# Optimization experiments

Measured on AMD Instinct MI355X. Metric: run time of the kernel, lower is better.

## Reference

```python
import jax, jax.numpy as jnp
import numpy as np

EMB = 1024
NH = 16
HS = EMB // NH

def setup_inputs() -> dict:
    key = jax.random.key(0)
    ks = jax.random.split(key, 9)
    s = 0.02
    x = jax.random.normal(ks[0], (4, 2048, EMB), dtype=jnp.float32)
    Wq = jax.random.normal(ks[1], (EMB, EMB), dtype=jnp.float32) * s
    bq = jnp.zeros((EMB,), jnp.float32)
    Wk = jax.random.normal(ks[2], (EMB, EMB), dtype=jnp.float32) * s
    bk = jnp.zeros((EMB,), jnp.float32)
    Wv = jax.random.normal(ks[3], (EMB, EMB), dtype=jnp.float32) * s
    bv = jnp.zeros((EMB,), jnp.float32)
    Wo = jax.random.normal(ks[4], (EMB, EMB), dtype=jnp.float32) * s
    bo = jnp.zeros((EMB,), jnp.float32)
    return {"x": x, "Wq": Wq, "bq": bq, "Wk": Wk, "bk": bk,
            "Wv": Wv, "bv": bv, "Wo": Wo, "bo": bo}

def reference(x, Wq, bq, Wk, bk, Wv, bv, Wo, bo):
    B, T, C = x.shape
    q = x @ Wq + bq
    k = x @ Wk + bk
    v = x @ Wv + bv
    # [B, H, T, hs]
    q = q.reshape(B, T, NH, HS).transpose(0, 2, 1, 3)
    k = k.reshape(B, T, NH, HS).transpose(0, 2, 1, 3)
    v = v.reshape(B, T, NH, HS).transpose(0, 2, 1, 3)
    scale = 1.0 / np.sqrt(HS).astype(np.float32)
    att = jnp.einsum('bhqd,bhkd->bhqk', q, k) * scale
    causal = jnp.tril(jnp.ones((T, T), dtype=bool))
    att = jnp.where(causal[None, None], att, jnp.float32(-jnp.inf))
    att = jax.nn.softmax(att, axis=-1)
    y = jnp.einsum('bhqk,bhkd->bhqd', att, v)
    y = y.transpose(0, 2, 1, 3).reshape(B, T, C)
    return y @ Wo + bo
```

## Files before the change

kernel.cpp:

```cpp
#include <hip/hip_runtime.h>

#define EMB   1024
#define NHEAD 16
#define HS    64
#define BATCH 4
#define SEQ   2048
#define MTOK  (BATCH*SEQ)

typedef __bf16 bf16;
typedef __bf16 bf16x8 __attribute__((ext_vector_type(8)));
typedef __bf16 bf16x4 __attribute__((ext_vector_type(4)));
typedef float  f32x4  __attribute__((ext_vector_type(4)));
typedef _Float16 f16;
typedef f16 f16x4 __attribute__((ext_vector_type(4)));
typedef f16 f16x8 __attribute__((ext_vector_type(8)));

#define MFMA16(a,b,c)     __builtin_amdgcn_mfma_f32_16x16x32_bf16(a,b,c,0,0,0)
#define MFMA_H32(a,b,c)   __builtin_amdgcn_mfma_f32_16x16x32_f16(a,b,c,0,0,0)
#define MFMA_H16(a,b,c)   __builtin_amdgcn_mfma_f32_16x16x16f16(a,b,c,0,0,0)

#if __has_builtin(__builtin_amdgcn_exp2f)
#define EXP2(x) __builtin_amdgcn_exp2f(x)
#else
#define EXP2(x) exp2f(x)
#endif

#define GLL(g, l) __builtin_amdgcn_global_load_lds(                         \
        (const __attribute__((address_space(1))) void*)(g),                 \
        (__attribute__((address_space(3))) void*)(l), 16, 0, 0)

__global__ __launch_bounds__(256) void k_prep(
        const float* __restrict__ x, bf16* __restrict__ xb,
        const float* __restrict__ W0, const float* __restrict__ W1,
        const float* __restrict__ W2, const float* __restrict__ W3,
        bf16* __restrict__ T0, bf16* __restrict__ T1,
        bf16* __restrict__ T2, bf16* __restrict__ T3) {
    const int z = blockIdx.z;
    if (z == 0) {
        const int blk = blockIdx.y * 16 + blockIdx.x;
        const size_t base = (size_t)blk * 32768;
        for (int j = threadIdx.x; j < 8192; j += 256) {
            size_t i = base + (size_t)j * 4;
            float4 v = *(const float4*)(x + i);
            bf16x4 o;
            o[0] = (bf16)v.x; o[1] = (bf16)v.y; o[2] = (bf16)v.z; o[3] = (bf16)v.w;
            *(bf16x4*)(xb + i) = o;
        }
        return;
    }
    __shared__ float tile[64][65];
    const float* W = (z == 1) ? W0 : (z == 2) ? W1 : (z == 3) ? W2 : W3;
    bf16* Wt = (z == 1) ? T0 : (z == 2) ? T1 : (z == 3) ? T2 : T3;
    int c0 = blockIdx.x * 64, r0 = blockIdx.y * 64;
    int tx = threadIdx.x & 63, ty = threadIdx.x >> 6;
    #pragma unroll
    for (int r = ty; r < 64; r += 4)
        tile[r][tx] = W[(r0 + r) * EMB + c0 + tx];
    __syncthreads();
    #pragma unroll
    for (int cc = ty; cc < 64; cc += 4)
        Wt[(c0 + cc) * EMB + r0 + tx] = (bf16)tile[tx][cc];
}

__global__ __launch_bounds__(512, 2) void k_qkv_gemm(
        const bf16* __restrict__ xb,
        const bf16* __restrict__ Wqt, const bf16* __restrict__ Wkt, const bf16* __restrict__ Wvt,
        const float* __restrict__ bq, const float* __restrict__ bk, const float* __restrict__ bv,
        f16* __restrict__ Q, f16* __restrict__ K, f16* __restrict__ Vt) {
    __shared__ __align__(16) bf16 As[4][8192];
    __shared__ __align__(16) bf16 Bs[4][8192];
    const int tid = threadIdx.x;
    const int lane = tid & 63;
    const int wave = tid >> 6;
    const int l15 = lane & 15, quad = lane >> 4;
    const int wm = wave >> 2;
    const int wn = wave & 3;

    const int bid = blockIdx.x;
    const int swz = (bid & 7) * 48 + (bid >> 3);
    const int mt = swz & 31;
    const int nt = swz >> 5;
    const int which = nt >> 2;
    const int n0 = (nt & 3) * 256;

    const bf16* Wt   = (which == 0) ? Wqt : (which == 1) ? Wkt : Wvt;
    const float* bias = (which == 0) ? bq : (which == 1) ? bk : bv;

    f32x4 acc[8][4];
    #pragma unroll
    for (int i = 0; i < 8; i++)
        #pragma unroll
        for (int j = 0; j < 4; j++) acc[i][j] = (f32x4){0.f, 0.f, 0.f, 0.f};

    const int P  = tid >> 3, s8 = tid & 7;
    const int c  = s8 ^ (P & 7);
    const int r_ = 2 * P + (c >> 2);
    const int kc = c & 3;
    const bf16* Asrc = xb + (size_t)(mt * 256 + r_) * EMB + kc * 8;
    const bf16* Bsrc = Wt + (size_t)(n0 + r_) * EMB + kc * 8;

#define QSTAGE(t, q) do {                                                   \
        GLL(Asrc + (t) * 32,                 &As[q][tid * 8]);              \
        GLL(Asrc + 128 * EMB + (t) * 32,     &As[q][tid * 8 + 4096]);       \
        GLL(Bsrc + (t) * 32,                 &Bs[q][tid * 8]);              \
        GLL(Bsrc + 128 * EMB + (t) * 32,     &Bs[q][tid * 8 + 4096]); } while (0)

    int aoff[8], boff[4];
    #pragma unroll
    for (int mf = 0; mf < 8; mf++) {
        int row = wm * 128 + mf * 16 + l15;
        int p = row >> 1;
        int slot = (((row & 1) << 2) | quad) ^ (p & 7);
        aoff[mf] = p * 64 + slot * 8;
    }
    #pragma unroll
    for (int nf = 0; nf < 4; nf++) {
        int row = wn * 64 + nf * 16 + l15;
        int p = row >> 1;
        int slot = (((row & 1) << 2) | quad) ^ (p & 7);
        boff[nf] = p * 64 + slot * 8;
    }

    QSTAGE(0, 0);
    QSTAGE(1, 1);

    #pragma unroll
    for (int t = 0; t < 32; t++) {
        if (t < 31) asm volatile("s_waitcnt vmcnt(4)" ::: "memory");
        else        asm volatile("s_waitcnt vmcnt(0)" ::: "memory");
        __builtin_amdgcn_s_barrier();
        asm volatile("" ::: "memory");

        const bf16* Ab = As[t & 3];
        const bf16* Bb = Bs[t & 3];
        bf16x8 a[8], b[4];
        #pragma unroll
        for (int mf = 0; mf < 8; mf++) a[mf] = *(const bf16x8*)(Ab + aoff[mf]);
        #pragma unroll
        for (int nf = 0; nf < 4; nf++) b[nf] = *(const bf16x8*)(Bb + boff[nf]);

        if (t + 2 < 32) QSTAGE(t + 2, (t + 2) & 3);

        __builtin_amdgcn_s_setprio(1);
        #pragma unroll
        for (int mf = 0; mf < 8; mf++)
            #pragma unroll
            for (int nf = 0; nf < 4; nf++)
                acc[mf][nf] = MFMA16(a[mf], b[nf], acc[mf][nf]);
        __builtin_amdgcn_s_setprio(0);
    }
#undef QSTAGE

    const float QSCALE = 0.18033688011112043f;
    #pragma unroll
    for (int nf = 0; nf < 4; nf++) {
        const int col = n0 + wn * 64 + nf * 16 + l15;
        const float bv_ = bias[col];
        const int h = col >> 6, d = col & 63;
        #pragma unroll
        for (int mf = 0; mf < 8; mf++) {
            #pragma unroll
            for (int r = 0; r < 4; r++) {
                const int row = mt * 256 + wm * 128 + mf * 16 + quad * 4 + r;
                const int b_ = row >> 11, tk = row & (SEQ - 1);
                const float val = acc[mf][nf][r] + bv_;
                if (which == 0) {
                    Q[((size_t)(b_ * NHEAD + h) * SEQ + tk) * HS + d] = (f16)(val * QSCALE);
                } else if (which == 1) {
                    K[((size_t)(b_ * NHEAD + h) * SEQ + tk) * HS + d] = (f16)val;
                } else {
                    Vt[(((size_t)(b_ * NHEAD + h) * 32 + (tk >> 6)) * 64 + d) * 64 + (tk & 63)] = (f16)val;
                }
            }
        }
    }
}

__global__ __launch_bounds__(256) void k_attn(
        const f16* __restrict__ Q, const f16* __restrict__ K,
        const f16* __restrict__ Vt, bf16* __restrict__ y) {
    __shared__ __align__(16) f16 kbuf[2][64 * 64];
    __shared__ __align__(16) f16 vbuf[2][64 * 64];
    const int tid = threadIdx.x;
    const int wave = tid >> 6, lane = tid & 63;
    const int l15 = lane & 15, quad = lane >> 4;
    const int qtA = blockIdx.x;
    const int bh = blockIdx.y;
    const int h = bh & (NHEAD - 1), b_ = bh >> 4;

    const f16* Qb = Q + (size_t)bh * SEQ * HS;
    const f16* Kb = K + (size_t)bh * SEQ * HS;
    const f16* Vb = Vt + (size_t)bh * 32 * 4096;

    const int c0 = tid, c1 = tid + 256;
    const int soff0 = (c0 >> 3) * 64 + (((c0 & 7) ^ ((c0 >> 3) & 7)) * 8);
    const int soff1 = (c1 >> 3) * 64 + (((c1 & 7) ^ ((c1 >> 3) & 7)) * 8);
    const int swz = l15 & 7;

    f16x4 ones;
    #pragma unroll
    for (int i = 0; i < 4; i++) ones[i] = (f16)1.0f;

    #pragma unroll 1
    for (int phase = 0; phase < 2; ++phase) {
        const int qt = phase ? (15 - qtA) : qtA;
        const int ntiles = 2 * qt + 2;
        const int qrow0 = qt * 128 + wave * 32;

        f16x8 qb[2][2];
        #pragma unroll
        for (int qf = 0; qf < 2; qf++)
            #pragma unroll
            for (int dk = 0; dk < 2; dk++)
                qb[qf][dk] = *(const f16x8*)(Qb + (qrow0 + 16 * qf + l15) * HS + 32 * dk + quad * 8);

        f32x4 o[2][4], lacc[2];
        #pragma unroll
        for (int qf = 0; qf < 2; qf++) {
            lacc[qf] = (f32x4){0.f, 0.f, 0.f, 0.f};
            #pragma unroll
            for (int df = 0; df < 4; df++) o[qf][df] = (f32x4){0.f, 0.f, 0.f, 0.f};
        }

        f16x8 kr0 = *(const f16x8*)(Kb + c0 * 8);
        f16x8 kr1 = *(const f16x8*)(Kb + c1 * 8);
        f16x8 vr0 = *(const f16x8*)(Vb + c0 * 8);
        f16x8 vr1 = *(const f16x8*)(Vb + c1 * 8);
        __syncthreads();
        *(f16x8*)(kbuf[0] + soff0) = kr0;
        *(f16x8*)(kbuf[0] + soff1) = kr1;
        *(f16x8*)(vbuf[0] + soff0) = vr0;
        *(f16x8*)(vbuf[0] + soff1) = vr1;

        for (int it = 0; it < ntiles; ++it) {
            const int kv0 = it * 64;
            __syncthreads();
            if (it + 1 < ntiles) {
                const f16* kg = Kb + (size_t)(kv0 + 64) * HS;
                const f16* vg = Vb + (size_t)(it + 1) * 4096;
                kr0 = *(const f16x8*)(kg + c0 * 8);
                kr1 = *(const f16x8*)(kg + c1 * 8);
                vr0 = *(const f16x8*)(vg + c0 * 8);
                vr1 = *(const f16x8*)(vg + c1 * 8);
            }
            if (kv0 <= qrow0 + 31) {
                const f16* kb_ = kbuf[it & 1];
                const f16* vb_ = vbuf[it & 1];

                f32x4 s[4][2];
                #pragma unroll
                for (int mb = 0; mb < 4; mb++) {
                    f16x8 ka0 = *(const f16x8*)(kb_ + (16 * mb + l15) * 64 + ((quad ^ swz) * 8));
                    f16x8 ka1 = *(const f16x8*)(kb_ + (16 * mb + l15) * 64 + (((4 + quad) ^ swz) * 8));
                    #pragma unroll
                    for (int qf = 0; qf < 2; qf++) {
                        f32x4 t = (f32x4){0.f, 0.f, 0.f, 0.f};
                        t = MFMA_H32(ka0, qb[qf][0], t);
                        t = MFMA_H32(ka1, qb[qf][1], t);
                        s[mb][qf] = t;
                    }
                }

                f16x4 pa[4][2];
                const bool edge = (kv0 + 63 > qrow0);
                #pragma unroll
                for (int mb = 0; mb < 4; mb++)
                    #pragma unroll
                    for (int qf = 0; qf < 2; qf++) {
                        f16x4 p;
                        if (edge) {
                            #pragma unroll
                            for (int r = 0; r < 4; r++) {
                                const int kvc = kv0 + 16 * mb + quad * 4 + r;
                                const int qq  = qrow0 + 16 * qf + l15;
                                p[r] = (f16)((kvc <= qq) ? EXP2(s[mb][qf][r]) : 0.f);
                            }
                        } else {
                            #pragma unroll
                            for (int r = 0; r < 4; r++)
                                p[r] = (f16)EXP2(s[mb][qf][r]);
                        }
                        pa[mb][qf] = p;
                    }

                #pragma unroll
                for (int df = 0; df < 4; df++)
                    #pragma unroll
                    for (int kb = 0; kb < 4; kb++) {
                        f16x4 vfrag = *(const f16x4*)(vb_ + (16 * df + l15) * 64 +
                                        (((2 * kb + (quad >> 1)) ^ swz) * 8) + (quad & 1) * 4);
                        #pragma unroll
                        for (int qf = 0; qf < 2; qf++)
                            o[qf][df] = MFMA_H16(pa[kb][qf], vfrag, o[qf][df]);
                    }
                #pragma unroll
                for (int kb = 0; kb < 4; kb++)
                    #pragma unroll
                    for (int qf = 0; qf < 2; qf++)
                        lacc[qf] = MFMA_H16(pa[kb][qf], ones, lacc[qf]);
            }
            if (it + 1 < ntiles) {
                const int nb = (it + 1) & 1;
                *(f16x8*)(kbuf[nb] + soff0) = kr0;
                *(f16x8*)(kbuf[nb] + soff1) = kr1;
                *(f16x8*)(vbuf[nb] + soff0) = vr0;
                *(f16x8*)(vbuf[nb] + soff1) = vr1;
            }
        }

        #pragma unroll
        for (int qf = 0; qf < 2; qf++)
            #pragma unroll
            for (int r = 0; r < 4; r++) {
                float inv = 1.f / lacc[qf][r];
                int t = qrow0 + 16 * qf + quad * 4 + r;
                bf16* yp = y + ((size_t)(b_ * SEQ + t)) * EMB + h * HS;
                #pragma unroll
                for (int df = 0; df < 4; df++)
                    yp[df * 16 + l15] = (bf16)(o[qf][df][r] * inv);
            }
    }
}

__global__ __launch_bounds__(256) void k_out_gemm(
        const bf16* __restrict__ y, const bf16* __restrict__ Wot,
        const float* __restrict__ bo, float* __restrict__ out) {
    __shared__ __align__(16) bf16 As[128 * 64];
    __shared__ __align__(16) bf16 Bs[128 * 64];
    const int tid = threadIdx.x;
    const int lane = tid & 63;
    const int wave = tid >> 6;
    const int l15 = lane & 15, quad = lane >> 4;
    const int wm = (wave >> 1) * 64, wn = (wave & 1) * 64;
    const int m0 = blockIdx.x * 128;
    const int n0 = blockIdx.y * 128;

    f32x4 acc[4][4];
    #pragma unroll
    for (int i = 0; i < 4; i++)
        #pragma unroll
        for (int j = 0; j < 4; j++) acc[i][j] = (f32x4){0.f, 0.f, 0.f, 0.f};

    const int r0_ = tid >> 3;
    const int kcs = ((tid & 7) ^ (r0_ & 7)) * 8;
    const bf16* Ag = y   + (size_t)m0 * EMB + r0_ * EMB + kcs;
    const bf16* Bg = Wot + (size_t)n0 * EMB + r0_ * EMB + kcs;
    const int rsw = l15 & 7;

    for (int k0 = 0; k0 < EMB; k0 += 64) {
        __syncthreads();
        #pragma unroll
        for (int g = 0; g < 4; g++) {
            GLL(Ag + 32 * g * EMB + k0, As + (tid + g * 256) * 8);
            GLL(Bg + 32 * g * EMB + k0, Bs + (tid + g * 256) * 8);
        }
        __syncthreads();

        bf16x8 af[2][4], bfr[2][4];
        #pragma unroll
        for (int h = 0; h < 2; h++) {
            #pragma unroll
            for (int rf = 0; rf < 4; rf++)
                af[h][rf] = *(const bf16x8*)(As + (wm + rf * 16 + l15) * 64 +
                                             (((4 * h + quad) ^ rsw) * 8));
            #pragma unroll
            for (int cf = 0; cf < 4; cf++)
                bfr[h][cf] = *(const bf16x8*)(Bs + (wn + cf * 16 + l15) * 64 +
                                              (((4 * h + quad) ^ rsw) * 8));
        }
        #pragma unroll
        for (int h = 0; h < 2; h++)
            #pragma unroll
            for (int rf = 0; rf < 4; rf++)
                #pragma unroll
                for (int cf = 0; cf < 4; cf++)
                    acc[rf][cf] = MFMA16(af[h][rf], bfr[h][cf], acc[rf][cf]);
    }

    #pragma unroll
    for (int cf = 0; cf < 4; cf++) {
        const int col = n0 + wn + cf * 16 + l15;
        const float bv_ = bo[col];
        #pragma unroll
        for (int rf = 0; rf < 4; rf++) {
            #pragma unroll
            for (int r = 0; r < 4; r++) {
                const int row = m0 + wm + rf * 16 + quad * 4 + r;
                out[(size_t)row * EMB + col] = acc[rf][cf][r] + bv_;
            }
        }
    }
}

extern "C" void kernel_launch(void* const* d_in, const int* in_sizes, int n_in,
                              void* d_out, int out_size, void* d_ws, size_t ws_size,
                              hipStream_t stream) {
    const float* x  = (const float*)d_in[0];
    const float* Wq = (const float*)d_in[1];
    const float* bq = (const float*)d_in[2];
    const float* Wk = (const float*)d_in[3];
    const float* bk = (const float*)d_in[4];
    const float* Wv = (const float*)d_in[5];
    const float* bv = (const float*)d_in[6];
    const float* Wo = (const float*)d_in[7];
    const float* bo = (const float*)d_in[8];
    float* out = (float*)d_out;

    char* ws = (char*)d_ws;
    bf16* xb  = (bf16*)(ws);
    bf16* Wqt = (bf16*)(ws + (16u << 20));
    bf16* Wkt = (bf16*)(ws + (18u << 20));
    bf16* Wvt = (bf16*)(ws + (20u << 20));
    bf16* Wot = (bf16*)(ws + (22u << 20));
    f16*  Q   = (f16*)(ws + (24u << 20));
    f16*  K   = (f16*)(ws + (40u << 20));
    f16*  Vt  = (f16*)(ws + (56u << 20));
    bf16* y   = (bf16*)(ws + (72u << 20));

    dim3 gp(16, 16, 5);
    k_prep<<<gp, 256, 0, stream>>>(x, xb, Wq, Wk, Wv, Wo, Wqt, Wkt, Wvt, Wot);

    dim3 g1(384);
    k_qkv_gemm<<<g1, 512, 0, stream>>>(xb, Wqt, Wkt, Wvt, bq, bk, bv, Q, K, Vt);

    dim3 g2(SEQ / 256, BATCH * NHEAD);
    k_attn<<<g2, 256, 0, stream>>>(Q, K, Vt, y);

    dim3 g3(MTOK / 128, EMB / 128);
    k_out_gemm<<<g3, 256, 0, stream>>>(y, Wot, bo, out);
}
```

Baseline: 322.9 us.

## Restructure QKV GEMM main loop into K=64 windows with interleaved MFMA/LDS schedule

The QKV projection GEMM now stages 64-wide K slices in a double buffer instead of 32-wide slices in a four-deep ring. Each window splits LDS fragment loads and MFMA groups into phases separated by barriers, priority hints and sched_barriers, with A and B prefetches issued at different points. The swizzled 1D grid becomes a plain 2D grid, and the V-transposed epilogue writes 4-element vectors instead of scalar stores. The aim is better overlap of global loads, LDS reads and matrix ops. The costs are more barriers per K step and the loss of the L2-friendly block swizzle.

```diff
diff --git a/kernel.cpp b/kernel.cpp
--- a/kernel.cpp
+++ b/kernel.cpp
@@ -67,89 +67,105 @@
         const bf16* __restrict__ Wqt, const bf16* __restrict__ Wkt, const bf16* __restrict__ Wvt,
         const float* __restrict__ bq, const float* __restrict__ bk, const float* __restrict__ bv,
         f16* __restrict__ Q, f16* __restrict__ K, f16* __restrict__ Vt) {
-    __shared__ __align__(16) bf16 As[4][8192];
-    __shared__ __align__(16) bf16 Bs[4][8192];
+    __shared__ __align__(16) bf16 As[2][256 * 64];
+    __shared__ __align__(16) bf16 Bs[2][256 * 64];
     const int tid = threadIdx.x;
     const int lane = tid & 63;
+    const int l15 = lane & 15, quad = lane >> 4;
     const int wave = tid >> 6;
-    const int l15 = lane & 15, quad = lane >> 4;
     const int wm = wave >> 2;
     const int wn = wave & 3;
 
-    const int bid = blockIdx.x;
-    const int swz = (bid & 7) * 48 + (bid >> 3);
-    const int mt = swz & 31;
-    const int nt = swz >> 5;
+    const int mt = blockIdx.x;
+    const int nt = blockIdx.y;
     const int which = nt >> 2;
     const int n0 = (nt & 3) * 256;
 
     const bf16* Wt   = (which == 0) ? Wqt : (which == 1) ? Wkt : Wvt;
     const float* bias = (which == 0) ? bq : (which == 1) ? bk : bv;
 
+    const bf16* Abase = xb + (size_t)mt * 256 * EMB;
+    const bf16* Bbase = Wt + (size_t)n0 * EMB;
+
+    const int srow = tid >> 3;
+    const int sc8  = ((tid & 7) ^ (srow & 7)) * 8;
+    const int sdst = srow * 64 + (tid & 7) * 8;
+
+    const int arow = (wm * 128 + l15) * 64;
+    const int brow = (wn * 64 + l15) * 64;
+    const int k7 = l15 & 7;
+    const int ksl0 = ((quad) ^ k7) * 8;
+    const int ksl1 = ((4 + quad) ^ k7) * 8;
+
     f32x4 acc[8][4];
     #pragma unroll
     for (int i = 0; i < 8; i++)
         #pragma unroll
         for (int j = 0; j < 4; j++) acc[i][j] = (f32x4){0.f, 0.f, 0.f, 0.f};
 
-    const int P  = tid >> 3, s8 = tid & 7;
-    const int c  = s8 ^ (P & 7);
-    const int r_ = 2 * P + (c >> 2);
-    const int kc = c & 3;
-    const bf16* Asrc = xb + (size_t)(mt * 256 + r_) * EMB + kc * 8;
-    const bf16* Bsrc = Wt + (size_t)(n0 + r_) * EMB + kc * 8;
-
-#define QSTAGE(t, q) do {                                                   \
-        GLL(Asrc + (t) * 32,                 &As[q][tid * 8]);              \
-        GLL(Asrc + 128 * EMB + (t) * 32,     &As[q][tid * 8 + 4096]);       \
-        GLL(Bsrc + (t) * 32,                 &Bs[q][tid * 8]);              \
-        GLL(Bsrc + 128 * EMB + (t) * 32,     &Bs[q][tid * 8 + 4096]); } while (0)
-
-    int aoff[8], boff[4];
-    #pragma unroll
-    for (int mf = 0; mf < 8; mf++) {
-        int row = wm * 128 + mf * 16 + l15;
-        int p = row >> 1;
-        int slot = (((row & 1) << 2) | quad) ^ (p & 7);
-        aoff[mf] = p * 64 + slot * 8;
-    }
-    #pragma unroll
-    for (int nf = 0; nf < 4; nf++) {
-        int row = wn * 64 + nf * 16 + l15;
-        int p = row >> 1;
-        int slot = (((row & 1) << 2) | quad) ^ (p & 7);
-        boff[nf] = p * 64 + slot * 8;
-    }
-
-    QSTAGE(0, 0);
-    QSTAGE(1, 1);
-
-    #pragma unroll
-    for (int t = 0; t < 32; t++) {
-        if (t < 31) asm volatile("s_waitcnt vmcnt(4)" ::: "memory");
-        else        asm volatile("s_waitcnt vmcnt(0)" ::: "memory");
-        __builtin_amdgcn_s_barrier();
-        asm volatile("" ::: "memory");
-
-        const bf16* Ab = As[t & 3];
-        const bf16* Bb = Bs[t & 3];
-        bf16x8 a[8], b[4];
-        #pragma unroll
-        for (int mf = 0; mf < 8; mf++) a[mf] = *(const bf16x8*)(Ab + aoff[mf]);
-        #pragma unroll
-        for (int nf = 0; nf < 4; nf++) b[nf] = *(const bf16x8*)(Bb + boff[nf]);
-
-        if (t + 2 < 32) QSTAGE(t + 2, (t + 2) & 3);
-
-        __builtin_amdgcn_s_setprio(1);
-        #pragma unroll
-        for (int mf = 0; mf < 8; mf++)
-            #pragma unroll
-            for (int nf = 0; nf < 4; nf++)
-                acc[mf][nf] = MFMA16(a[mf], b[nf], acc[mf][nf]);
-        __builtin_amdgcn_s_setprio(0);
-    }
-#undef QSTAGE
+#define STAGE_A(T, cb) do { const int ko = (T) * 64;                          \
+    GLL(Abase + (size_t)(srow      ) * EMB + ko + sc8, &As[cb][sdst        ]);\
+    GLL(Abase + (size_t)(srow +  64) * EMB + ko + sc8, &As[cb][sdst + 4096 ]);\
+    GLL(Abase + (size_t)(srow + 128) * EMB + ko + sc8, &As[cb][sdst + 8192 ]);\
+    GLL(Abase + (size_t)(srow + 192) * EMB + ko + sc8, &As[cb][sdst + 12288]);\
+} while (0)
+#define STAGE_B(T, cb) do { const int ko = (T) * 64;                          \
+    GLL(Bbase + (size_t)(srow      ) * EMB + ko + sc8, &Bs[cb][sdst        ]);\
+    GLL(Bbase + (size_t)(srow +  64) * EMB + ko + sc8, &Bs[cb][sdst + 4096 ]);\
+    GLL(Bbase + (size_t)(srow + 128) * EMB + ko + sc8, &Bs[cb][sdst + 8192 ]);\
+    GLL(Bbase + (size_t)(srow + 192) * EMB + ko + sc8, &Bs[cb][sdst + 12288]);\
+} while (0)
+
+#define LDA(c_, mf, ks) (*(const bf16x8*)(&As[c_][arow + (mf) * 1024 + (ks)]))
+#define LDB(c_, nf, ks) (*(const bf16x8*)(&Bs[c_][brow + (nf) * 1024 + (ks)]))
+
+#define BARX __builtin_amdgcn_s_barrier()
+#define PRI1 __builtin_amdgcn_s_setprio(1)
+#define PRI0 __builtin_amdgcn_s_setprio(0)
+#define SCHB __builtin_amdgcn_sched_barrier(0)
+#define VM4 asm volatile("s_waitcnt vmcnt(4)" ::: "memory")
+#define VM0 asm volatile("s_waitcnt vmcnt(0)" ::: "memory")
+
+#define MF4(mb, av)                                                          \
+    _Pragma("unroll") for (int i_ = 0; i_ < 4; i_++)                         \
+    _Pragma("unroll") for (int j_ = 0; j_ < 4; j_++)                         \
+        acc[(mb) + i_][j_] = MFMA16(av[i_], br[j_], acc[(mb) + i_][j_])
+
+#define WINDOW(c_, SA, SB, VM) do {                                          \
+    _Pragma("unroll") for (int i = 0; i < 4; i++) ar[i]  = LDA(c_, i,     ksl0);\
+    _Pragma("unroll") for (int j = 0; j < 4; j++) br[j]  = LDB(c_, j,     ksl0);\
+    SA;                                                                      \
+    SCHB;                                                                    \
+    BARX; PRI1; MF4(0, ar);  PRI0; BARX;                                     \
+    _Pragma("unroll") for (int i = 0; i < 4; i++) ar2[i] = LDA(c_, 4 + i, ksl0);\
+    BARX; PRI1; MF4(4, ar2); PRI0; BARX;                                     \
+    _Pragma("unroll") for (int i = 0; i < 4; i++) ar[i]  = LDA(c_, i,     ksl1);\
+    _Pragma("unroll") for (int j = 0; j < 4; j++) br[j]  = LDB(c_, j,     ksl1);\
+    BARX; PRI1; MF4(0, ar);  PRI0; BARX;                                     \
+    _Pragma("unroll") for (int i = 0; i < 4; i++) ar2[i] = LDA(c_, 4 + i, ksl1);\
+    SB;                                                                      \
+    SCHB; VM;                                                                \
+    BARX; PRI1; MF4(4, ar2); PRI0; BARX;                                     \
+} while (0)
+
+    STAGE_A(0, 0); STAGE_B(0, 0); STAGE_B(1, 1);
+    SCHB;
+    VM4;
+    BARX;
+
+    bf16x8 ar[4], br[4], ar2[4];
+    #pragma unroll 2
+    for (int W = 0; W < 14; ++W) {
+        const int c = W & 1;
+        WINDOW(c, STAGE_A(W + 1, c ^ 1), STAGE_B(W + 2, c), VM4);
+    }
+    WINDOW(0, STAGE_A(15, 1), (void)0, VM0);
+    WINDOW(1, (void)0, (void)0, (void)0);
+
+#undef WINDOW
+#undef MF4
+#undef STAGE_A
+#undef STAGE_B
 
     const float QSCALE = 0.18033688011112043f;
     #pragma unroll
@@ -159,18 +175,24 @@
         const int h = col >> 6, d = col & 63;
         #pragma unroll
         for (int mf = 0; mf < 8; mf++) {
-            #pragma unroll
-            for (int r = 0; r < 4; r++) {
-                const int row = mt * 256 + wm * 128 + mf * 16 + quad * 4 + r;
-                const int b_ = row >> 11, tk = row & (SEQ - 1);
-                const float val = acc[mf][nf][r] + bv_;
-                if (which == 0) {
-                    Q[((size_t)(b_ * NHEAD + h) * SEQ + tk) * HS + d] = (f16)(val * QSCALE);
-                } else if (which == 1) {
-                    K[((size_t)(b_ * NHEAD + h) * SEQ + tk) * HS + d] = (f16)val;
-                } else {
-                    Vt[(((size_t)(b_ * NHEAD + h) * 32 + (tk >> 6)) * 64 + d) * 64 + (tk & 63)] = (f16)val;
-                }
+            const int row0 = mt * 256 + wm * 128 + mf * 16 + quad * 4;
+            const int b_ = row0 >> 11, tk0 = row0 & (SEQ - 1);
+            if (which == 0) {
+                #pragma unroll
+                for (int r = 0; r < 4; r++)
+                    Q[((size_t)(b_ * NHEAD + h) * SEQ + (tk0 + r)) * HS + d] =
+                        (f16)((acc[mf][nf][r] + bv_) * QSCALE);
+            } else if (which == 1) {
+                #pragma unroll
+                for (int r = 0; r < 4; r++)
+                    K[((size_t)(b_ * NHEAD + h) * SEQ + (tk0 + r)) * HS + d] =
+                        (f16)(acc[mf][nf][r] + bv_);
+            } else {
+                f16x4 vv;
+                #pragma unroll
+                for (int r = 0; r < 4; r++) vv[r] = (f16)(acc[mf][nf][r] + bv_);
+                *(f16x4*)(Vt + (((size_t)(b_ * NHEAD + h) * 32 + (tk0 >> 6)) * 64 + d) * 64
+                          + (tk0 & 63)) = vv;
             }
         }
     }
@@ -420,7 +442,7 @@
     dim3 gp(16, 16, 5);
     k_prep<<<gp, 256, 0, stream>>>(x, xb, Wq, Wk, Wv, Wo, Wqt, Wkt, Wvt, Wot);
 
-    dim3 g1(384);
+    dim3 g1(32, 12);
     k_qkv_gemm<<<g1, 512, 0, stream>>>(xb, Wqt, Wkt, Wvt, bq, bk, bv, Q, K, Vt);
 
     dim3 g2(SEQ / 256, BATCH * NHEAD);
```

Result: faster. 287.4 us (-11.0%).

## Restructure QKV GEMM pipeline into double-buffered split-phase schedule with vectorized stores

Applied to the files above, without the earlier changes.

Replaces the 4-deep LDS ring (prefetch distance 2) in the QKV GEMM with a 2-buffer scheme. Each k-step is split into two MFMA halves, with the A and B global-to-LDS loads for the next step interleaved between them and separated by barriers and scheduling fences. The swizzled 1D block mapping becomes a plain 2D grid, which may reduce L2 locality. The epilogue is specialized per output: V^T gets vectorized f16x4 stores, and Q/K use a shared scaled path. Less LDS per block could raise occupancy, but the shallower prefetch and full vmcnt(0) waits each step risk exposing memory latency.

```diff
diff --git a/kernel.cpp b/kernel.cpp
--- a/kernel.cpp
+++ b/kernel.cpp
@@ -67,110 +67,154 @@
         const bf16* __restrict__ Wqt, const bf16* __restrict__ Wkt, const bf16* __restrict__ Wvt,
         const float* __restrict__ bq, const float* __restrict__ bk, const float* __restrict__ bv,
         f16* __restrict__ Q, f16* __restrict__ K, f16* __restrict__ Vt) {
-    __shared__ __align__(16) bf16 As[4][8192];
-    __shared__ __align__(16) bf16 Bs[4][8192];
+    __shared__ __align__(16) bf16 As[2][8192];
+    __shared__ __align__(16) bf16 Bs[2][8192];
     const int tid = threadIdx.x;
     const int lane = tid & 63;
+    const int l15 = lane & 15, quad = lane >> 4;
     const int wave = tid >> 6;
-    const int l15 = lane & 15, quad = lane >> 4;
     const int wm = wave >> 2;
     const int wn = wave & 3;
 
-    const int bid = blockIdx.x;
-    const int swz = (bid & 7) * 48 + (bid >> 3);
-    const int mt = swz & 31;
-    const int nt = swz >> 5;
+    const int mt = blockIdx.x;
+    const int nt = blockIdx.y;
     const int which = nt >> 2;
     const int n0 = (nt & 3) * 256;
 
     const bf16* Wt   = (which == 0) ? Wqt : (which == 1) ? Wkt : Wvt;
     const float* bias = (which == 0) ? bq : (which == 1) ? bk : bv;
 
+    const bf16* Abase = xb + (size_t)mt * 256 * EMB;
+    const bf16* Bbase = Wt + (size_t)n0 * EMB;
+
+    const int P   = tid >> 3, s8 = tid & 7;
+    const int cch = s8 ^ (P & 7);
+    const int r_  = 2 * P + (cch >> 2);
+    const int kc8 = (cch & 3) * 8;
+    const bf16* Asrc = Abase + (size_t)r_ * EMB + kc8;
+    const bf16* Bsrc = Bbase + (size_t)r_ * EMB + kc8;
+
+#define STAGE_A(T, cb) do {                                                  \
+    GLL(Asrc + (T) * 32,             &As[cb][tid * 8]);                      \
+    GLL(Asrc + 128 * EMB + (T) * 32, &As[cb][tid * 8 + 4096]); } while (0)
+#define STAGE_B(T, cb) do {                                                  \
+    GLL(Bsrc + (T) * 32,             &Bs[cb][tid * 8]);                      \
+    GLL(Bsrc + 128 * EMB + (T) * 32, &Bs[cb][tid * 8 + 4096]); } while (0)
+
+    int aoff[8], boff[4];
+    #pragma unroll
+    for (int mf = 0; mf < 8; mf++) {
+        const int row = wm * 128 + mf * 16 + l15;
+        const int Pr = row >> 1, hh = row & 1;
+        aoff[mf] = Pr * 64 + ((((hh << 2) | quad)) ^ (Pr & 7)) * 8;
+    }
+    #pragma unroll
+    for (int nf = 0; nf < 4; nf++) {
+        const int row = wn * 64 + nf * 16 + l15;
+        const int Pr = row >> 1, hh = row & 1;
+        boff[nf] = Pr * 64 + ((((hh << 2) | quad)) ^ (Pr & 7)) * 8;
+    }
+
     f32x4 acc[8][4];
     #pragma unroll
     for (int i = 0; i < 8; i++)
         #pragma unroll
         for (int j = 0; j < 4; j++) acc[i][j] = (f32x4){0.f, 0.f, 0.f, 0.f};
 
-    const int P  = tid >> 3, s8 = tid & 7;
-    const int c  = s8 ^ (P & 7);
-    const int r_ = 2 * P + (c >> 2);
-    const int kc = c & 3;
-    const bf16* Asrc = xb + (size_t)(mt * 256 + r_) * EMB + kc * 8;
-    const bf16* Bsrc = Wt + (size_t)(n0 + r_) * EMB + kc * 8;
-
-#define QSTAGE(t, q) do {                                                   \
-        GLL(Asrc + (t) * 32,                 &As[q][tid * 8]);              \
-        GLL(Asrc + 128 * EMB + (t) * 32,     &As[q][tid * 8 + 4096]);       \
-        GLL(Bsrc + (t) * 32,                 &Bs[q][tid * 8]);              \
-        GLL(Bsrc + 128 * EMB + (t) * 32,     &Bs[q][tid * 8 + 4096]); } while (0)
-
-    int aoff[8], boff[4];
-    #pragma unroll
-    for (int mf = 0; mf < 8; mf++) {
-        int row = wm * 128 + mf * 16 + l15;
-        int p = row >> 1;
-        int slot = (((row & 1) << 2) | quad) ^ (p & 7);
-        aoff[mf] = p * 64 + slot * 8;
-    }
-    #pragma unroll
-    for (int nf = 0; nf < 4; nf++) {
-        int row = wn * 64 + nf * 16 + l15;
-        int p = row >> 1;
-        int slot = (((row & 1) << 2) | quad) ^ (p & 7);
-        boff[nf] = p * 64 + slot * 8;
-    }
-
-    QSTAGE(0, 0);
-    QSTAGE(1, 1);
-
-    #pragma unroll
-    for (int t = 0; t < 32; t++) {
-        if (t < 31) asm volatile("s_waitcnt vmcnt(4)" ::: "memory");
-        else        asm volatile("s_waitcnt vmcnt(0)" ::: "memory");
-        __builtin_amdgcn_s_barrier();
-        asm volatile("" ::: "memory");
-
-        const bf16* Ab = As[t & 3];
-        const bf16* Bb = Bs[t & 3];
-        bf16x8 a[8], b[4];
-        #pragma unroll
-        for (int mf = 0; mf < 8; mf++) a[mf] = *(const bf16x8*)(Ab + aoff[mf]);
-        #pragma unroll
-        for (int nf = 0; nf < 4; nf++) b[nf] = *(const bf16x8*)(Bb + boff[nf]);
-
-        if (t + 2 < 32) QSTAGE(t + 2, (t + 2) & 3);
-
-        __builtin_amdgcn_s_setprio(1);
-        #pragma unroll
-        for (int mf = 0; mf < 8; mf++)
-            #pragma unroll
-            for (int nf = 0; nf < 4; nf++)
-                acc[mf][nf] = MFMA16(a[mf], b[nf], acc[mf][nf]);
-        __builtin_amdgcn_s_setprio(0);
-    }
-#undef QSTAGE
+#define BARX __builtin_amdgcn_s_barrier()
+#define PRI1 __builtin_amdgcn_s_setprio(1)
+#define PRI0 __builtin_amdgcn_s_setprio(0)
+#define SCHB __builtin_amdgcn_sched_barrier(0)
+#define VM0 asm volatile("s_waitcnt vmcnt(0)" ::: "memory")
+
+    STAGE_A(0, 0); STAGE_B(0, 0);
+    SCHB; VM0; BARX;
+
+    bf16x8 a[4], b[4], a2[4];
+    #pragma unroll 1
+    for (int W = 0; W < 31; ++W) {
+        const int c = W & 1;
+        const bf16* Ab = As[c];
+        const bf16* Bb = Bs[c];
+        #pragma unroll
+        for (int i = 0; i < 4; i++) a[i] = *(const bf16x8*)(Ab + aoff[i]);
+        #pragma unroll
+        for (int j = 0; j < 4; j++) b[j] = *(const bf16x8*)(Bb + boff[j]);
+        STAGE_A(W + 1, c ^ 1);
+        SCHB;
+        BARX; PRI1;
+        #pragma unroll
+        for (int i = 0; i < 4; i++)
+            #pragma unroll
+            for (int j = 0; j < 4; j++)
+                acc[i][j] = MFMA16(a[i], b[j], acc[i][j]);
+        PRI0;
+        #pragma unroll
+        for (int i = 0; i < 4; i++) a2[i] = *(const bf16x8*)(Ab + aoff[4 + i]);
+        STAGE_B(W + 1, c ^ 1);
+        SCHB; VM0; BARX;
+        PRI1;
+        #pragma unroll
+        for (int i = 0; i < 4; i++)
+            #pragma unroll
+            for (int j = 0; j < 4; j++)
+                acc[4 + i][j] = MFMA16(a2[i], b[j], acc[4 + i][j]);
+        PRI0;
+    }
+    {
+        const bf16* Ab = As[1];
+        const bf16* Bb = Bs[1];
+        #pragma unroll
+        for (int i = 0; i < 4; i++) a[i] = *(const bf16x8*)(Ab + aoff[i]);
+        #pragma unroll
+        for (int j = 0; j < 4; j++) b[j] = *(const bf16x8*)(Bb + boff[j]);
+        #pragma unroll
+        for (int i = 0; i < 4; i++) a2[i] = *(const bf16x8*)(Ab + aoff[4 + i]);
+        #pragma unroll
+        for (int i = 0; i < 4; i++)
+            #pragma unroll
+            for (int j = 0; j < 4; j++) {
+                acc[i][j]     = MFMA16(a[i],  b[j], acc[i][j]);
+                acc[4 + i][j] = MFMA16(a2[i], b[j], acc[4 + i][j]);
+            }
+    }
+#undef STAGE_A
+#undef STAGE_B
 
     const float QSCALE = 0.18033688011112043f;
-    #pragma unroll
-    for (int nf = 0; nf < 4; nf++) {
-        const int col = n0 + wn * 64 + nf * 16 + l15;
-        const float bv_ = bias[col];
-        const int h = col >> 6, d = col & 63;
+    const int h = (n0 >> 6) + wn;
+    if (which == 2) {
+        #pragma unroll
+        for (int nf = 0; nf < 4; nf++) {
+            const float bv_ = bias[n0 + wn * 64 + nf * 16 + l15];
+            const int d = nf * 16 + l15;
+            #pragma unroll
+            for (int mf = 0; mf < 8; mf++) {
+                const int row0 = mt * 256 + wm * 128 + mf * 16 + quad * 4;
+                const int b_ = row0 >> 11, tk0 = row0 & (SEQ - 1);
+                f16x4 vv;
+                #pragma unroll
+                for (int r = 0; r < 4; r++) vv[r] = (f16)(acc[mf][nf][r] + bv_);
+                *(f16x4*)(Vt + (((size_t)(b_ * NHEAD + h) * 32 + (tk0 >> 6)) * 64 + d) * 64
+                          + (tk0 & 63)) = vv;
+            }
+        }
+    } else {
+        f16* OUT = (which == 0) ? Q : K;
+        const float scl = (which == 0) ? QSCALE : 1.0f;
+        float bvv[4];
+        #pragma unroll
+        for (int nf = 0; nf < 4; nf++) bvv[nf] = bias[n0 + wn * 64 + nf * 16 + l15];
         #pragma unroll
         for (int mf = 0; mf < 8; mf++) {
+            const int row0 = mt * 256 + wm * 128 + mf * 16 + quad * 4;
+            const int b_ = row0 >> 11, tk0 = row0 & (SEQ - 1);
             #pragma unroll
             for (int r = 0; r < 4; r++) {
-                const int row = mt * 256 + wm * 128 + mf * 16 + quad * 4 + r;
-                const int b_ = row >> 11, tk = row & (SEQ - 1);
-                const float val = acc[mf][nf][r] + bv_;
-                if (which == 0) {
-                    Q[((size_t)(b_ * NHEAD + h) * SEQ + tk) * HS + d] = (f16)(val * QSCALE);
-                } else if (which == 1) {
-                    K[((size_t)(b_ * NHEAD + h) * SEQ + tk) * HS + d] = (f16)val;
-                } else {
-                    Vt[(((size_t)(b_ * NHEAD + h) * 32 + (tk >> 6)) * 64 + d) * 64 + (tk & 63)] = (f16)val;
-                }
+                f16* op = OUT + ((size_t)(b_ * NHEAD + h) * SEQ + (tk0 + r)) * HS + l15;
+                #pragma unroll
+                for (int nf = 0; nf < 4; nf++)
+                    op[nf * 16] = (f16)((acc[mf][nf][r] + bvv[nf]) * scl);
             }
         }
     }
@@ -420,7 +464,7 @@
     dim3 gp(16, 16, 5);
     k_prep<<<gp, 256, 0, stream>>>(x, xb, Wq, Wk, Wv, Wo, Wqt, Wkt, Wvt, Wot);
 
-    dim3 g1(384);
+    dim3 g1(32, 12);
     k_qkv_gemm<<<g1, 512, 0, stream>>>(xb, Wqt, Wkt, Wvt, bq, bk, bv, Q, K, Vt);
 
     dim3 g2(SEQ / 256, BATCH * NHEAD);
```

After: 286.1 us. 1.13x faster.
